# Kernel optimization log

Hardware: AMD Instinct MI355X
Metric: run time of the kernel (lower is better)

Reference implementation:

```python
import jax, jax.numpy as jnp
import numpy as np

MARGIN = 0.3
EPS = 1e-12


def setup_inputs() -> dict:
    key = jax.random.key(0)
    k1, k2, k3 = jax.random.split(key, 3)
    B, D = 8192, 1024
    features = jax.random.normal(k1, (B, D), dtype=jnp.float32)
    labels = jax.random.randint(k2, (B,), 0, 100, dtype=jnp.int64)
    domain_labels = jax.random.randint(k3, (B,), 0, 2, dtype=jnp.int64)
    return {"features": features, "labels": labels, "domain_labels": domain_labels}


def reference(features, labels, domain_labels):
    # L2-normalize rows (F.normalize: x / max(||x||, eps))
    norm = jnp.maximum(jnp.linalg.norm(features, axis=1, keepdims=True), EPS)
    f = features / norm

    herb = domain_labels == 0   # [B] anchors
    field = domain_labels == 1  # [B] candidates

    sq = jnp.sum(f * f, axis=1)                                   # [B]
    d2 = sq[:, None] + sq[None, :] - 2.0 * jnp.einsum('id,jd->ij', f, f)
    d = jnp.sqrt(jnp.maximum(d2, 0.0))                            # [B, B]

    same = labels[:, None] == labels[None, :]                     # [B, B]
    pair = herb[:, None] & field[None, :]
    pos_mask = pair & same
    neg_mask = pair & ~same

    INF = jnp.float32(jnp.inf)
    pos_min = jnp.min(jnp.where(pos_mask, d, INF), axis=1)        # [B]
    neg_min = jnp.min(jnp.where(neg_mask, d, INF), axis=1)        # [B]

    valid = herb & jnp.any(pos_mask, axis=1) & jnp.any(neg_mask, axis=1)
    # Substitute 0 for invalid rows BEFORE subtracting to avoid inf - inf.
    pos_s = jnp.where(valid, pos_min, 0.0)
    neg_s = jnp.where(valid, neg_min, 0.0)
    tl = jnp.maximum(pos_s - neg_s + MARGIN, 0.0)                 # [B]

    loss_sum = jnp.sum(jnp.where(valid, tl, 0.0))
    count = jnp.sum(valid.astype(jnp.float32))
    return jnp.where(count > 0, loss_sum / jnp.maximum(count, 1.0), 0.0)
```

## Files before the change

### kernel.cpp

```cpp
#include <hip/hip_runtime.h>


#define B_ROWS 8192
#define DIM    1024

typedef __bf16 bf16x8 __attribute__((ext_vector_type(8)));
typedef float  f32x4  __attribute__((ext_vector_type(4)));

__device__ __forceinline__ unsigned short f2bf_rne(float x) {
    unsigned u = __float_as_uint(x);
    unsigned r = (u + 0x7FFFu + ((u >> 16) & 1u)) >> 16;
    return (unsigned short)r;
}
__device__ __forceinline__ float bf2f(unsigned short h) {
    return __uint_as_float(((unsigned)h) << 16);
}

__device__ __forceinline__ void async_copy16(const void* g, void* l) {
    __builtin_amdgcn_global_load_lds(
        (const __attribute__((address_space(1))) unsigned int*)g,
        (__attribute__((address_space(3))) unsigned int*)l,
        16, 0, 0);
}

__global__ __launch_bounds__(256) void compute_slots(
    const int* __restrict__ dom, int* __restrict__ slotOf,
    unsigned* __restrict__ cnt)
{
    __shared__ int cnts[256];
    __shared__ int base[257];
    const int t = threadIdx.x;
    const int p0 = t * 32;

    unsigned mask = 0u; int c = 0;
    #pragma unroll
    for (int i = 0; i < 32; ++i) {
        const int isA = (dom[p0 + i] == 0) ? 1 : 0;
        mask |= ((unsigned)isA) << i;
        c += isA;
    }
    cnts[t] = c;
    __syncthreads();
    if (t == 0) {
        int acc = 0;
        for (int i = 0; i < 256; ++i) { base[i] = acc; acc += cnts[i]; }
        base[256] = acc;
        cnt[0] = (unsigned)acc;
    }
    __syncthreads();
    const int nA = base[256];
    int aB = base[t];
    #pragma unroll
    for (int i = 0; i < 32; ++i) {
        const int isA = (mask >> i) & 1;
        slotOf[p0 + i] = isA ? aB : nA + (p0 + i - aB);
        aB += isA;
    }
}

__global__ __launch_bounds__(256) void normalize_rows(
    const float* __restrict__ feat, const int* __restrict__ labels,
    const int* __restrict__ slotOf, unsigned short* __restrict__ G,
    int* __restrict__ labG, float* __restrict__ sqG)
{
    const int wv = threadIdx.x >> 6, lane = threadIdx.x & 63;
    const int row = blockIdx.x * 4 + wv;

    const float4* src = (const float4*)(feat + (size_t)row * DIM);
    float4 v[4];
    float ss = 0.0f;
    #pragma unroll
    for (int j = 0; j < 4; ++j) {
        v[j] = src[j * 64 + lane];
        ss += v[j].x * v[j].x + v[j].y * v[j].y + v[j].z * v[j].z + v[j].w * v[j].w;
    }
    #pragma unroll
    for (int s = 32; s > 0; s >>= 1) ss += __shfl_xor(ss, s);
    const float inv = 1.0f / fmaxf(sqrtf(ss), 1e-12f);

    const int slot = slotOf[row];
    unsigned short ub[16];
    float ss2 = 0.0f;
    #pragma unroll
    for (int j = 0; j < 4; ++j) {
        const float f0 = v[j].x * inv, f1 = v[j].y * inv,
                    f2 = v[j].z * inv, f3 = v[j].w * inv;
        ub[j * 4 + 0] = f2bf_rne(f0); ub[j * 4 + 1] = f2bf_rne(f1);
        ub[j * 4 + 2] = f2bf_rne(f2); ub[j * 4 + 3] = f2bf_rne(f3);
        #pragma unroll
        for (int q = 0; q < 4; ++q) {
            const float fr = bf2f(ub[j * 4 + q]);
            ss2 += fr * fr;
        }
    }
    #pragma unroll
    for (int s = 32; s > 0; s >>= 1) ss2 += __shfl_xor(ss2, s);
    if (lane == 0) {
        sqG[slot]  = ss2;
        labG[slot] = labels[row];
    }
    ushort4* dst = (ushort4*)(G + (size_t)slot * DIM);
    #pragma unroll
    for (int j = 0; j < 4; ++j) {
        ushort4 pk;
        pk.x = ub[j * 4 + 0]; pk.y = ub[j * 4 + 1];
        pk.z = ub[j * 4 + 2]; pk.w = ub[j * 4 + 3];
        dst[j * 64 + lane] = pk;
    }
}

__global__ __launch_bounds__(256) void tile_mindist(
    const unsigned short* __restrict__ G, const int* __restrict__ labG,
    const float* __restrict__ sqG, const unsigned* __restrict__ cnt,
    unsigned* __restrict__ posmin, unsigned* __restrict__ negmin)
{
    const int nA = (int)cnt[0];
    const int nF = B_ROWS - nA;
    const int nTA = (nA + 127) >> 7;
    const int nTF = (nF + 127) >> 7;
    if (nTA == 0 || nTF == 0) return;

    const int strip = (nTF + 7) >> 3;
    const int xcd  = blockIdx.x & 7;
    const int slot = blockIdx.x >> 3;
    const int tyBase = xcd * strip;
    const int nloc = nTA * strip;

    __shared__ __align__(16) unsigned short S[2][2][128 * 32];

    const int t = threadIdx.x;
    const int lane = t & 63, w = t >> 6;
    const int wm = w >> 1, wn = w & 1;
    const int l15 = lane & 15, quad = lane >> 4;

    const int ch0 = 2 * w;
    const int crow = lane >> 2;
    const int cbyte = (lane & 3) * 16;

    const int rdA = (wm * 64 + l15) * 32 + quad * 8;
    const int rdF = (wn * 64 + l15) * 32 + quad * 8;

    const char* Gb = (const char*)G;

    for (int idx = slot; idx < nloc; idx += 132) {
        const int ty = tyBase + idx / nTA;
        if (ty >= nTF) break;
        const int tx = idx % nTA;
        const int rowA0 = tx * 128;
        const int rowF0 = nA + ty * 128;

        const char* ga[2]; const char* gf[2];
        #pragma unroll
        for (int h = 0; h < 2; ++h) {
            const int ch = ch0 + h;
            const int rA = rowA0 + 16 * ch + crow;
            int rF = rowF0 + 16 * ch + crow;
            if (rF > B_ROWS - 1) rF = B_ROWS - 1;
            ga[h] = Gb + (size_t)rA * (DIM * 2) + cbyte;
            gf[h] = Gb + (size_t)rF * (DIM * 2) + cbyte;
        }

        f32x4 acc[4][4] = {};

        #pragma unroll
        for (int h = 0; h < 2; ++h) {
            async_copy16(ga[h], &S[0][0][(ch0 + h) * 512]);
            async_copy16(gf[h], &S[0][1][(ch0 + h) * 512]);
        }
        __syncthreads();

        #pragma unroll 4
        for (int step = 0; step < 32; ++step) {
            const int cur = step & 1;
            const int nb = cur ^ 1;
            if (step < 31) {
                const int off = (step + 1) * 64;
                #pragma unroll
                for (int h = 0; h < 2; ++h) {
                    async_copy16(ga[h] + off, &S[nb][0][(ch0 + h) * 512]);
                    async_copy16(gf[h] + off, &S[nb][1][(ch0 + h) * 512]);
                }
            }

            const unsigned short* pa = &S[cur][0][rdA];
            const unsigned short* pf = &S[cur][1][rdF];
            bf16x8 a[4], b[4];
            #pragma unroll
            for (int fm = 0; fm < 4; ++fm) a[fm] = *(const bf16x8*)(pa + fm * 512);
            #pragma unroll
            for (int fn = 0; fn < 4; ++fn) b[fn] = *(const bf16x8*)(pf + fn * 512);
            #pragma unroll
            for (int fm = 0; fm < 4; ++fm)
                #pragma unroll
                for (int fn = 0; fn < 4; ++fn)
                    acc[fm][fn] = __builtin_amdgcn_mfma_f32_16x16x32_bf16(
                        a[fm], b[fn], acc[fm][fn], 0, 0, 0);

            __syncthreads();
        }

        const float INFV = __uint_as_float(0x7f800000u);
        float sqf[4]; int lf_[4]; bool vf[4];
        #pragma unroll
        for (int fn = 0; fn < 4; ++fn) {
            const int rf = rowF0 + wn * 64 + fn * 16 + l15;
            vf[fn] = rf < B_ROWS;
            const int rc = vf[fn] ? rf : (B_ROWS - 1);
            sqf[fn] = sqG[rc];
            lf_[fn] = labG[rc];
        }
        #pragma unroll
        for (int fm = 0; fm < 4; ++fm) {
            #pragma unroll
            for (int r = 0; r < 4; ++r) {
                const int ra = rowA0 + wm * 64 + fm * 16 + quad * 4 + r;
                const bool va = ra < nA;
                const int rac = va ? ra : 0;
                const float sqa = sqG[rac];
                const int la_ = labG[rac];
                float pmin = INFV, nmin = INFV;
                #pragma unroll
                for (int fn = 0; fn < 4; ++fn) {
                    const float dd = fmaxf(sqa + sqf[fn] - 2.0f * acc[fm][fn][r], 0.0f);
                    if (vf[fn]) {
                        if (la_ == lf_[fn]) pmin = fminf(pmin, dd);
                        else                nmin = fminf(nmin, dd);
                    }
                }
                #pragma unroll
                for (int s = 1; s < 16; s <<= 1) {
                    pmin = fminf(pmin, __shfl_xor(pmin, s));
                    nmin = fminf(nmin, __shfl_xor(nmin, s));
                }
                if (l15 == 0 && va) {
                    if (pmin < INFV) atomicMin(&posmin[ra], __float_as_uint(pmin));
                    if (nmin < INFV) atomicMin(&negmin[ra], __float_as_uint(nmin));
                }
            }
        }
        __syncthreads();
    }
}

__global__ __launch_bounds__(256) void reduce_one(
    const unsigned* __restrict__ posmin, const unsigned* __restrict__ negmin,
    float* __restrict__ out)
{
    const int t = threadIdx.x;
    const int lane = t & 63, w = t >> 6;
    float tl = 0.0f, c = 0.0f;
    #pragma unroll
    for (int j = 0; j < 32; ++j) {
        const int i = j * 256 + t;
        const unsigned up = posmin[i], un = negmin[i];
        if (up != 0xFFFFFFFFu && un != 0xFFFFFFFFu) {
            const float pd = sqrtf(__uint_as_float(up));
            const float nd = sqrtf(__uint_as_float(un));
            tl += fmaxf(pd - nd + 0.3f, 0.0f);
            c += 1.0f;
        }
    }
    #pragma unroll
    for (int s = 32; s > 0; s >>= 1) {
        tl += __shfl_down(tl, s);
        c  += __shfl_down(c, s);
    }
    __shared__ float sb[8];
    if (lane == 0) { sb[w] = tl; sb[4 + w] = c; }
    __syncthreads();
    if (t == 0) {
        const float s = sb[0] + sb[1] + sb[2] + sb[3];
        const float cc = sb[4] + sb[5] + sb[6] + sb[7];
        out[0] = (cc > 0.0f) ? s / fmaxf(cc, 1.0f) : 0.0f;
    }
}

extern "C" void kernel_launch(void* const* d_in, const int* in_sizes, int n_in,
                              void* d_out, int out_size, void* d_ws, size_t ws_size,
                              hipStream_t stream) {
    const float* feat  = (const float*)d_in[0];
    const int* labels  = (const int*)d_in[1];
    const int* dom     = (const int*)d_in[2];
    float* out = (float*)d_out;

    char* ws = (char*)d_ws;
    unsigned short* G   = (unsigned short*)(ws);
    int*      labG      = (int*)(ws + 16777216);
    float*    sqG       = (float*)(ws + 16809984);
    unsigned* posmin    = (unsigned*)(ws + 16842752);
    unsigned* negmin    = (unsigned*)(ws + 16875520);
    unsigned* cnt       = (unsigned*)(ws + 16908288);
    int*      slotOf    = (int*)(ws + 16842752);

    compute_slots<<<1, 256, 0, stream>>>(dom, slotOf, cnt);
    normalize_rows<<<B_ROWS / 4, 256, 0, stream>>>(feat, labels, slotOf,
                                                   G, labG, sqG);

    hipMemsetAsync(posmin, 0xFF, 65536, stream);

    tile_mindist<<<1056, 256, 0, stream>>>(G, labG, sqG, cnt, posmin, negmin);

    reduce_one<<<1, 256, 0, stream>>>(posmin, negmin, out);
}
```

Baseline: 182.9 us.

## Fuse slot computation into normalize and enlarge anchor tile to 256 rows

Removes the single-block compute_slots kernel: every normalize block now recomputes the domain prefix counts in shared memory and derives each row's slot with a popcount, saving one launch and the slotOf round trip. The min-distance kernel tile grows from 128x128 to 256x128 anchor-by-candidate, so each wave holds 8x4 MFMA accumulators, raising arithmetic intensity per LDS load. The grid drops to 768 blocks with a stride of 96. The cost is more register pressure and LDS per block, which may lower occupancy, plus every normalize block redundantly scanning the whole domain array.

New measurement: 250.6 us. 1.37x slower.

```diff
diff --git a/kernel.cpp b/kernel.cpp
--- a/kernel.cpp
+++ b/kernel.cpp
@@ -23,48 +23,43 @@
         16, 0, 0);
 }
 
-__global__ __launch_bounds__(256) void compute_slots(
-    const int* __restrict__ dom, int* __restrict__ slotOf,
-    unsigned* __restrict__ cnt)
+__global__ __launch_bounds__(256) void normalize_rows(
+    const float* __restrict__ feat, const int* __restrict__ labels,
+    const int* __restrict__ dom, unsigned short* __restrict__ G,
+    int* __restrict__ labG, float* __restrict__ sqG, unsigned* __restrict__ cnt)
 {
     __shared__ int cnts[256];
     __shared__ int base[257];
+    __shared__ unsigned masks[256];
     const int t = threadIdx.x;
-    const int p0 = t * 32;
-
-    unsigned mask = 0u; int c = 0;
-    #pragma unroll
-    for (int i = 0; i < 32; ++i) {
-        const int isA = (dom[p0 + i] == 0) ? 1 : 0;
-        mask |= ((unsigned)isA) << i;
-        c += isA;
-    }
-    cnts[t] = c;
+
+    {
+        unsigned mask = 0u; int c = 0;
+        #pragma unroll
+        for (int i = 0; i < 32; ++i) {
+            const int isA = (dom[t * 32 + i] == 0) ? 1 : 0;
+            mask |= ((unsigned)isA) << i;
+            c += isA;
+        }
+        cnts[t] = c; masks[t] = mask;
+    }
     __syncthreads();
     if (t == 0) {
         int acc = 0;
         for (int i = 0; i < 256; ++i) { base[i] = acc; acc += cnts[i]; }
         base[256] = acc;
-        cnt[0] = (unsigned)acc;
+        if (blockIdx.x == 0) cnt[0] = (unsigned)acc;
     }
     __syncthreads();
+
+    const int wv = t >> 6, lane = t & 63;
+    const int row = blockIdx.x * 4 + wv;
     const int nA = base[256];
-    int aB = base[t];
-    #pragma unroll
-    for (int i = 0; i < 32; ++i) {
-        const int isA = (mask >> i) & 1;
-        slotOf[p0 + i] = isA ? aB : nA + (p0 + i - aB);
-        aB += isA;
-    }
-}
-
-__global__ __launch_bounds__(256) void normalize_rows(
-    const float* __restrict__ feat, const int* __restrict__ labels,
-    const int* __restrict__ slotOf, unsigned short* __restrict__ G,
-    int* __restrict__ labG, float* __restrict__ sqG)
-{
-    const int wv = threadIdx.x >> 6, lane = threadIdx.x & 63;
-    const int row = blockIdx.x * 4 + wv;
+    const int chunk = row >> 5, bit = row & 31;
+    const unsigned m = masks[chunk];
+    const int aBefore = base[chunk] + __popc(m & ((bit ? (1u << bit) : 1u) - 1u));
+    const int isA = (m >> bit) & 1;
+    const int slot = isA ? aBefore : nA + (row - aBefore);
 
     const float4* src = (const float4*)(feat + (size_t)row * DIM);
     float4 v[4];
@@ -78,7 +73,6 @@
     for (int s = 32; s > 0; s >>= 1) ss += __shfl_xor(ss, s);
     const float inv = 1.0f / fmaxf(sqrtf(ss), 1e-12f);
 
-    const int slot = slotOf[row];
     unsigned short ub[16];
     float ss2 = 0.0f;
     #pragma unroll
@@ -116,7 +110,7 @@
 {
     const int nA = (int)cnt[0];
     const int nF = B_ROWS - nA;
-    const int nTA = (nA + 127) >> 7;
+    const int nTA = (nA + 255) >> 8;
     const int nTF = (nF + 127) >> 7;
     if (nTA == 0 || nTF == 0) return;
 
@@ -126,47 +120,50 @@
     const int tyBase = xcd * strip;
     const int nloc = nTA * strip;
 
-    __shared__ __align__(16) unsigned short S[2][2][128 * 32];
+    __shared__ __align__(16) unsigned short SA[2][256 * 32];
+    __shared__ __align__(16) unsigned short SF[2][128 * 32];
 
     const int t = threadIdx.x;
     const int lane = t & 63, w = t >> 6;
-    const int wm = w >> 1, wn = w & 1;
+    const int wm2 = w >> 1, wn = w & 1;
     const int l15 = lane & 15, quad = lane >> 4;
 
-    const int ch0 = 2 * w;
     const int crow = lane >> 2;
     const int cbyte = (lane & 3) * 16;
 
-    const int rdA = (wm * 64 + l15) * 32 + quad * 8;
+    const int rdA = (wm2 * 128 + l15) * 32 + quad * 8;
     const int rdF = (wn * 64 + l15) * 32 + quad * 8;
 
     const char* Gb = (const char*)G;
 
-    for (int idx = slot; idx < nloc; idx += 132) {
+    for (int idx = slot; idx < nloc; idx += 96) {
         const int ty = tyBase + idx / nTA;
         if (ty >= nTF) break;
         const int tx = idx % nTA;
-        const int rowA0 = tx * 128;
+        const int rowA0 = tx * 256;
         const int rowF0 = nA + ty * 128;
 
-        const char* ga[2]; const char* gf[2];
+        const char* ga[4]; const char* gf[2];
+        #pragma unroll
+        for (int h = 0; h < 4; ++h) {
+            const int rA = rowA0 + 16 * (4 * w + h) + crow;
+            ga[h] = Gb + (size_t)rA * (DIM * 2) + cbyte;
+        }
         #pragma unroll
         for (int h = 0; h < 2; ++h) {
-            const int ch = ch0 + h;
-            const int rA = rowA0 + 16 * ch + crow;
-            int rF = rowF0 + 16 * ch + crow;
+            int rF = rowF0 + 16 * (2 * w + h) + crow;
             if (rF > B_ROWS - 1) rF = B_ROWS - 1;
-            ga[h] = Gb + (size_t)rA * (DIM * 2) + cbyte;
             gf[h] = Gb + (size_t)rF * (DIM * 2) + cbyte;
         }
 
-        f32x4 acc[4][4] = {};
-
-        #pragma unroll
-        for (int h = 0; h < 2; ++h) {
-            async_copy16(ga[h], &S[0][0][(ch0 + h) * 512]);
-            async_copy16(gf[h], &S[0][1][(ch0 + h) * 512]);
-        }
+        f32x4 acc[8][4] = {};
+
+        #pragma unroll
+        for (int h = 0; h < 4; ++h)
+            async_copy16(ga[h], &SA[0][(4 * w + h) * 512]);
+        #pragma unroll
+        for (int h = 0; h < 2; ++h)
+            async_copy16(gf[h], &SF[0][(2 * w + h) * 512]);
         __syncthreads();
 
         #pragma unroll 4
@@ -176,21 +173,22 @@
             if (step < 31) {
                 const int off = (step + 1) * 64;
                 #pragma unroll
-                for (int h = 0; h < 2; ++h) {
-                    async_copy16(ga[h] + off, &S[nb][0][(ch0 + h) * 512]);
-                    async_copy16(gf[h] + off, &S[nb][1][(ch0 + h) * 512]);
-                }
+                for (int h = 0; h < 4; ++h)
+                    async_copy16(ga[h] + off, &SA[nb][(4 * w + h) * 512]);
+                #pragma unroll
+                for (int h = 0; h < 2; ++h)
+                    async_copy16(gf[h] + off, &SF[nb][(2 * w + h) * 512]);
             }
 
-            const unsigned short* pa = &S[cur][0][rdA];
-            const unsigned short* pf = &S[cur][1][rdF];
-            bf16x8 a[4], b[4];
+            bf16x8 a[8], b[4];
             #pragma unroll
-            for (int fm = 0; fm < 4; ++fm) a[fm] = *(const bf16x8*)(pa + fm * 512);
+            for (int fm = 0; fm < 8; ++fm)
+                a[fm] = *(const bf16x8*)(&SA[cur][rdA + fm * 512]);
             #pragma unroll
-            for (int fn = 0; fn < 4; ++fn) b[fn] = *(const bf16x8*)(pf + fn * 512);
+            for (int fn = 0; fn < 4; ++fn)
+                b[fn] = *(const bf16x8*)(&SF[cur][rdF + fn * 512]);
             #pragma unroll
-            for (int fm = 0; fm < 4; ++fm)
+            for (int fm = 0; fm < 8; ++fm)
                 #pragma unroll
                 for (int fn = 0; fn < 4; ++fn)
                     acc[fm][fn] = __builtin_amdgcn_mfma_f32_16x16x32_bf16(
@@ -210,10 +208,10 @@
             lf_[fn] = labG[rc];
         }
         #pragma unroll
-        for (int fm = 0; fm < 4; ++fm) {
+        for (int fm = 0; fm < 8; ++fm) {
             #pragma unroll
             for (int r = 0; r < 4; ++r) {
-                const int ra = rowA0 + wm * 64 + fm * 16 + quad * 4 + r;
+                const int ra = rowA0 + wm2 * 128 + fm * 16 + quad * 4 + r;
                 const bool va = ra < nA;
                 const int rac = va ? ra : 0;
                 const float sqa = sqG[rac];
@@ -290,15 +288,13 @@
     unsigned* posmin    = (unsigned*)(ws + 16842752);
     unsigned* negmin    = (unsigned*)(ws + 16875520);
     unsigned* cnt       = (unsigned*)(ws + 16908288);
-    int*      slotOf    = (int*)(ws + 16842752);
-
-    compute_slots<<<1, 256, 0, stream>>>(dom, slotOf, cnt);
-    normalize_rows<<<B_ROWS / 4, 256, 0, stream>>>(feat, labels, slotOf,
-                                                   G, labG, sqG);
+
+    normalize_rows<<<B_ROWS / 4, 256, 0, stream>>>(feat, labels, dom,
+                                                   G, labG, sqG, cnt);
 
     hipMemsetAsync(posmin, 0xFF, 65536, stream);
 
-    tile_mindist<<<1056, 256, 0, stream>>>(G, labG, sqG, cnt, posmin, negmin);
+    tile_mindist<<<768, 256, 0, stream>>>(G, labG, sqG, cnt, posmin, negmin);
 
     reduce_one<<<1, 256, 0, stream>>>(posmin, negmin, out);
 }
```
